# Performance work log

Measured on AMD Instinct MI355X. Metric: run time of the kernel, lower is better.

## Reference

```python
import jax, jax.numpy as jnp
import numpy as np

SCALE = 64 ** (-0.5)  # dim_head**-0.5; heads/dim_head otherwise unused in forward


def setup_inputs() -> dict:
    key = jax.random.key(0)
    ks = jax.random.split(key, 7)
    B, C, T = 8, 512, 4096
    s = C ** (-0.5)  # conv1d default init scale-ish
    x = jax.random.normal(ks[0], (B, C, T), dtype=jnp.float32)
    Wq = jax.random.normal(ks[1], (C, C), dtype=jnp.float32) * s
    bq = jax.random.normal(ks[2], (C,), dtype=jnp.float32) * s
    Wk = jax.random.normal(ks[3], (C, C), dtype=jnp.float32) * s
    bk = jax.random.normal(ks[4], (C,), dtype=jnp.float32) * s
    Wv = jax.random.normal(ks[5], (C, C), dtype=jnp.float32) * s
    bv = jax.random.normal(ks[6], (C,), dtype=jnp.float32) * s
    return {"x": x, "Wq": Wq, "bq": bq, "Wk": Wk, "bk": bk, "Wv": Wv, "bv": bv}


def reference(x, Wq, bq, Wk, bk, Wv, bv):
    # 1x1 Conv1d == per-timestep linear over channels: (o,c) x (b,c,t) -> (b,o,t)
    q = jnp.einsum('oc,bct->bot', Wq, x) + bq[None, :, None]
    k = jnp.einsum('oc,bct->bot', Wk, x) + bk[None, :, None]
    v = jnp.einsum('oc,bct->bot', Wv, x) + bv[None, :, None]
    # Channel-channel attention: dots (b, C, C); softmax over last (channel) axis
    dots = jnp.einsum('bct,bdt->bcd', q, k) * SCALE
    attn = jax.nn.softmax(dots, axis=-1)
    # (b,C,C) x (b,C,t) -> (b,C,t); dropout p=0 and to_out unused in original forward
    out = jnp.einsum('bcd,bdt->bct', attn, v)
    return out
```

## Files before the change

kernel.cpp:

```cpp
#include <hip/hip_runtime.h>

#define B_ 8
#define C_ 512
#define T_ 4096

typedef __attribute__((ext_vector_type(8))) __bf16 bf16x8;
typedef __attribute__((ext_vector_type(8))) _Float16 f16x8;
typedef __attribute__((ext_vector_type(8))) unsigned short u16x8;
typedef __attribute__((ext_vector_type(4))) float f32x4;

__device__ __forceinline__ unsigned short f2bf(float f) {
  unsigned int u = __float_as_uint(f);
  u += 0x7fffu + ((u >> 16) & 1u);
  return (unsigned short)(u >> 16);
}
__device__ __forceinline__ float bf2f(unsigned short h) {
  return __uint_as_float(((unsigned int)h) << 16);
}
__device__ __forceinline__ unsigned short f2h(float f) {
  return __builtin_bit_cast(unsigned short, (_Float16)f);
}

__device__ __forceinline__ void async16(unsigned short* ldsdst, const unsigned short* gsrc) {
  __builtin_amdgcn_global_load_lds(
      (__attribute__((address_space(1))) void*)(void*)const_cast<unsigned short*>(gsrc),
      (__attribute__((address_space(3))) void*)(void*)ldsdst,
      16, 0, 0);
}

template <bool F16>
__device__ __forceinline__ f32x4 mfma16(u16x8 a, u16x8 b, f32x4 c) {
  if constexpr (F16)
    return __builtin_amdgcn_mfma_f32_16x16x32_f16(
        __builtin_bit_cast(f16x8, a), __builtin_bit_cast(f16x8, b), c, 0, 0, 0);
  else
    return __builtin_amdgcn_mfma_f32_16x16x32_bf16(
        __builtin_bit_cast(bf16x8, a), __builtin_bit_cast(bf16x8, b), c, 0, 0, 0);
}

struct GemmP {
  const unsigned short* Ah; const unsigned short* Al; long sA; int lda;
  const unsigned short* Bh; const unsigned short* Bl; long sB; int ldb;
  float* Cf; unsigned short* Ch; unsigned short* Cl; long sC; int ldc;
  int kspan; int zparts;
  const float* rowv; const float* colv; const float* bq; const float* bk;
};

enum { EPI_F32 = 0, EPI_OUT = 1, EPI_DOTS = 2, EPI_SPLIT = 3, EPI_F16 = 4 };

template <int BM, int BN, int WM, int WN, bool SA, bool SB, int EPI, bool F16, bool TRI>
__global__ __launch_bounds__((BM / WM) * (BN / WN) * 64) void gemm_nt(GemmP g) {
  constexpr int KC = 64;
  constexpr int NWAVE = (BM / WM) * (BN / WN);
  constexpr int NT = NWAVE * 64;
  constexpr int ASZ = BM * KC, BSZ = BN * KC;
  constexpr int STAGE = (SA ? 2 : 1) * ASZ + (SB ? 2 : 1) * BSZ;
  constexpr int EPAD = BN + 4;
  constexpr int EPIB = 32 * EPAD * 4;
  constexpr int LDSB = (STAGE * 2 > EPIB) ? STAGE * 2 : EPIB;
  __shared__ alignas(16) char ldsraw[LDSB];
  unsigned short* lds = (unsigned short*)ldsraw;
  unsigned short* ldsAh = lds;
  unsigned short* ldsAl = lds + ASZ;
  unsigned short* ldsBh = lds + (SA ? 2 : 1) * ASZ;
  unsigned short* ldsBl = ldsBh + BSZ;

  const int tid = threadIdx.x;
  const int lane = tid & 63, wid = tid >> 6;
  constexpr int WNB = BN / WN;
  const int wm = wid / WNB, wn = wid % WNB;
  constexpr int MF = WM / 16, NF = WN / 16;

  int bm, bn;
  if constexpr (TRI) {
    const int t = blockIdx.x;
    const int tm = (t >= 6) ? 3 : (t >= 3) ? 2 : (t >= 1) ? 1 : 0;
    bm = tm; bn = t - (tm * (tm + 1)) / 2;
  } else {
    bm = blockIdx.x; bn = blockIdx.y;
  }
  const int z = blockIdx.z;
  const int b = z / g.zparts, kp = z - b * g.zparts;

  const unsigned short* Ah = g.Ah + (size_t)b * g.sA + (size_t)kp * g.kspan;
  const unsigned short* Al = SA ? (g.Al + (size_t)b * g.sA + (size_t)kp * g.kspan) : nullptr;
  const unsigned short* Bh = g.Bh + (size_t)b * g.sB + (size_t)kp * g.kspan;
  const unsigned short* Bl = SB ? (g.Bl + (size_t)b * g.sB + (size_t)kp * g.kspan) : nullptr;

  f32x4 acc[MF][NF] = {};

  const int kIters = g.kspan / KC;
  for (int kt = 0; kt < kIters; ++kt) {
    const int kb = kt * KC;
#pragma unroll
    for (int r = 0; r < ASZ / (8 * NT); ++r) {
      int idx = tid + r * NT;
      int row = idx >> 3, sl = idx & 7;
      int kc = (sl ^ (row & 7)) << 3;
      size_t goff = (size_t)(bm * BM + row) * g.lda + kb + kc;
      async16(&ldsAh[idx << 3], Ah + goff);
      if constexpr (SA) async16(&ldsAl[idx << 3], Al + goff);
    }
#pragma unroll
    for (int r = 0; r < BSZ / (8 * NT); ++r) {
      int idx = tid + r * NT;
      int row = idx >> 3, sl = idx & 7;
      int kc = (sl ^ (row & 7)) << 3;
      size_t goff = (size_t)(bn * BN + row) * g.ldb + kb + kc;
      async16(&ldsBh[idx << 3], Bh + goff);
      if constexpr (SB) async16(&ldsBl[idx << 3], Bl + goff);
    }
    __syncthreads();

    const int rsel = lane & 15, kq = lane >> 4;
#pragma unroll
    for (int ks = 0; ks < KC; ks += 32) {
      const int chunk = (ks >> 3) + kq;
      u16x8 afh[MF], afl[MF], bfh[NF], bfl[NF];
#pragma unroll
      for (int fm = 0; fm < MF; ++fm) {
        int row = wm * WM + fm * 16 + rsel;
        int ro = row * KC + ((chunk ^ (row & 7)) << 3);
        afh[fm] = *(const u16x8*)&ldsAh[ro];
        if constexpr (SA) afl[fm] = *(const u16x8*)&ldsAl[ro];
      }
#pragma unroll
      for (int fn = 0; fn < NF; ++fn) {
        int row = wn * WN + fn * 16 + rsel;
        int ro = row * KC + ((chunk ^ (row & 7)) << 3);
        bfh[fn] = *(const u16x8*)&ldsBh[ro];
        if constexpr (SB) bfl[fn] = *(const u16x8*)&ldsBl[ro];
      }
#pragma unroll
      for (int fm = 0; fm < MF; ++fm)
#pragma unroll
        for (int fn = 0; fn < NF; ++fn) {
          acc[fm][fn] = mfma16<F16>(afh[fm], bfh[fn], acc[fm][fn]);
          if constexpr (SB) acc[fm][fn] = mfma16<F16>(afh[fm], bfl[fn], acc[fm][fn]);
          if constexpr (SA) acc[fm][fn] = mfma16<F16>(afl[fm], bfh[fn], acc[fm][fn]);
        }
    }
    __syncthreads();
  }

  if constexpr (EPI == EPI_SPLIT || EPI == EPI_F16) {
#pragma unroll
    for (int fm = 0; fm < MF; ++fm)
#pragma unroll
      for (int fn = 0; fn < NF; ++fn)
#pragma unroll
        for (int r = 0; r < 4; ++r) {
          int i = bm * BM + wm * WM + fm * 16 + ((lane >> 4) << 2) + r;
          int j = bn * BN + wn * WN + fn * 16 + (lane & 15);
          float v = acc[fm][fn][r];
          size_t co = (size_t)z * g.sC + (size_t)i * g.ldc + j;
          if constexpr (EPI == EPI_SPLIT) {
            unsigned short h = f2bf(v);
            g.Ch[co] = h;
            g.Cl[co] = f2bf(v - bf2f(h));
          } else {
            g.Ch[co] = f2h(v);
          }
        }
  } else {
    float* eb = (float*)ldsraw;
#pragma unroll
    for (int ck = 0; ck < BM / 32; ++ck) {
      if (wm == (ck * 32) / WM) {
        const int fm0 = ((ck * 32) % WM) / 16;
#pragma unroll
        for (int fi = 0; fi < 2; ++fi) {
          int fm = fm0 + fi;
#pragma unroll
          for (int fn = 0; fn < NF; ++fn)
#pragma unroll
            for (int r = 0; r < 4; ++r) {
              int lrow = fi * 16 + ((lane >> 4) << 2) + r;
              int col = wn * WN + fn * 16 + (lane & 15);
              eb[lrow * EPAD + col] = acc[fm][fn][r];
            }
        }
      }
      __syncthreads();
#pragma unroll
      for (int it = 0; it < (32 * BN / 4) / NT; ++it) {
        int idx = it * NT + tid;
        int row = idx / (BN / 4), c4 = (idx % (BN / 4)) * 4;
        f32x4 v = *(f32x4*)&eb[row * EPAD + c4];
        int grow = bm * BM + ck * 32 + row;
        int j = bn * BN + c4;
        if constexpr (EPI == EPI_OUT) v = v + g.rowv[b * C_ + grow];
        if constexpr (EPI == EPI_DOTS) {
          f32x4 bkv = *(const f32x4*)&g.bk[j];
          f32x4 ksv = *(const f32x4*)&g.colv[b * C_ + j];
          float qsi = g.rowv[b * C_ + grow], bqi = g.bq[grow];
          v = 0.125f * (v + qsi * bkv + bqi * (ksv + 4096.f * bkv));
        }
        *(f32x4*)&g.Cf[(size_t)z * g.sC + (size_t)grow * g.ldc + j] = v;
      }
      __syncthreads();
    }
  }
}

#define NXB (64 * 8 * 8)
#define PAD 66
__global__ __launch_bounds__(256) void prep_fused(
    const float* __restrict__ x, const float* __restrict__ Wq,
    const float* __restrict__ Wk, const float* __restrict__ Wv,
    unsigned short* __restrict__ Xh, unsigned short* __restrict__ XhT,
    float* __restrict__ S, unsigned short* Wqh, unsigned short* Wql,
    unsigned short* Wkh, unsigned short* Wkl, unsigned short* WvT) {
  __shared__ unsigned short tile[64 * PAD];
  const int tid = threadIdx.x;
  if (blockIdx.x < NXB) {
    const int tl = blockIdx.x;
    const int t0 = (tl & 63) << 6, c0 = ((tl >> 6) & 7) << 6, b = tl >> 9;
    const float* xin = x + ((size_t)(b * C_ + c0)) * T_ + t0;
    unsigned short* xo = Xh + ((size_t)(b * C_ + c0)) * T_ + t0;
#pragma unroll
    for (int r = 0; r < 4; ++r) {
      int p = tid + r * 256;
      int row = p >> 4, c4 = (p & 15) << 2;
      float4 v = *(const float4*)&xin[(size_t)row * T_ + c4];
      unsigned short h0 = f2h(v.x), h1 = f2h(v.y), h2 = f2h(v.z), h3 = f2h(v.w);
      ushort4 hv; hv.x = h0; hv.y = h1; hv.z = h2; hv.w = h3;
      *(ushort4*)&xo[(size_t)row * T_ + c4] = hv;
      unsigned int lo = (unsigned int)h0 | ((unsigned int)h1 << 16);
      unsigned int hi = (unsigned int)h2 | ((unsigned int)h3 << 16);
      ((unsigned int*)&tile[row * PAD + c4])[0] = lo;
      ((unsigned int*)&tile[row * PAD + c4])[1] = hi;
      float s = v.x + v.y + v.z + v.w;
#pragma unroll
      for (int o = 1; o < 16; o <<= 1) s += __shfl_xor(s, o);
      if ((tid & 15) == 0) atomicAdd(&S[b * C_ + c0 + row], s);
    }
    __syncthreads();
#pragma unroll
    for (int r = 0; r < 2; ++r) {
      int idx = tid + r * 256;
      int trow = idx >> 3, cc = (idx & 7) << 3;
      unsigned short vals[8];
#pragma unroll
      for (int j = 0; j < 8; ++j) vals[j] = tile[(cc + j) * PAD + trow];
      *(uint4*)&XhT[((size_t)b * T_ + t0 + trow) * C_ + c0 + cc] = *(uint4*)vals;
    }
  } else {
    int i = (blockIdx.x - NXB) * 256 + tid;
    float q = Wq[i]; unsigned short qh = f2bf(q); Wqh[i] = qh; Wql[i] = f2bf(q - bf2f(qh));
    float k = Wk[i]; unsigned short kh = f2bf(k); Wkh[i] = kh; Wkl[i] = f2bf(k - bf2f(kh));
    float v = Wv[i]; int d = i >> 9, e = i & 511;
    WvT[(e << 9) + d] = f2h(v);
  }
}

__global__ __launch_bounds__(256) void combine_g(const float* __restrict__ gp,
                                                 unsigned short* __restrict__ gh,
                                                 unsigned short* __restrict__ gl) {
  __shared__ float tile[64 * 65];
  const int blk = blockIdx.x;
  const int b = blk >> 6, tr = (blk >> 3) & 7, tc = blk & 7;
  const bool mirror = (tr >> 1) < (tc >> 1);
  const int sr = mirror ? tc : tr, sc = mirror ? tr : tc;
  const float* src = gp + ((size_t)b << 21) + (size_t)(sr << 6) * 512 + (sc << 6);
  const int row = threadIdx.x >> 4, c4 = (threadIdx.x & 15) << 2;
  float vals[4][4];
#pragma unroll
  for (int rr = 0; rr < 4; ++rr) {
    const int r = row + rr * 16;
    f32x4 v = {};
#pragma unroll
    for (int p = 0; p < 8; ++p)
      v += *(const f32x4*)&src[((size_t)p << 18) + (size_t)r * 512 + c4];
    if (mirror) {
#pragma unroll
      for (int k = 0; k < 4; ++k) tile[r * 65 + c4 + k] = v[k];
    } else {
#pragma unroll
      for (int k = 0; k < 4; ++k) vals[rr][k] = v[k];
    }
  }
  if (mirror) {
    __syncthreads();
#pragma unroll
    for (int rr = 0; rr < 4; ++rr) {
      const int r = row + rr * 16;
#pragma unroll
      for (int k = 0; k < 4; ++k) vals[rr][k] = tile[(c4 + k) * 65 + r];
    }
  }
  unsigned short* ghp = gh + ((size_t)b << 18) + (size_t)(tr << 6) * 512 + (tc << 6);
  unsigned short* glp = gl + ((size_t)b << 18) + (size_t)(tr << 6) * 512 + (tc << 6);
#pragma unroll
  for (int rr = 0; rr < 4; ++rr) {
    const int r = row + rr * 16;
    ushort4 h, l;
    h.x = f2bf(vals[rr][0]); l.x = f2bf(vals[rr][0] - bf2f(h.x));
    h.y = f2bf(vals[rr][1]); l.y = f2bf(vals[rr][1] - bf2f(h.y));
    h.z = f2bf(vals[rr][2]); l.z = f2bf(vals[rr][2] - bf2f(h.z));
    h.w = f2bf(vals[rr][3]); l.w = f2bf(vals[rr][3] - bf2f(h.w));
    *(ushort4*)&ghp[(size_t)r * 512 + c4] = h;
    *(ushort4*)&glp[(size_t)r * 512 + c4] = l;
  }
}

__global__ __launch_bounds__(256) void qs_ks(const float* __restrict__ Wq, const float* __restrict__ Wk,
                                             const float* __restrict__ s, float* __restrict__ qs,
                                             float* __restrict__ ks) {
  int lane = threadIdx.x & 63, wid = threadIdx.x >> 6;
  int gi = blockIdx.x * 4 + wid;
  int b = gi >> 9, i = gi & 511;
  const float* sv = s + (b << 9);
  const float* wqr = Wq + (size_t)i * C_;
  const float* wkr = Wk + (size_t)i * C_;
  float aq = 0.f, ak = 0.f;
#pragma unroll
  for (int c = lane; c < C_; c += 64) {
    float sc = sv[c];
    aq += wqr[c] * sc;
    ak += wkr[c] * sc;
  }
#pragma unroll
  for (int o = 32; o > 0; o >>= 1) { aq += __shfl_down(aq, o); ak += __shfl_down(ak, o); }
  if (lane == 0) { qs[gi] = aq; ks[gi] = ak; }
}

__global__ __launch_bounds__(256) void softmax_rows(const float* __restrict__ logits,
                                                    const float* __restrict__ bv,
                                                    unsigned short* __restrict__ attn,
                                                    float* __restrict__ ab) {
  const int row = blockIdx.x;
  const int tid = threadIdx.x, lane = tid & 63, wid = tid >> 6;
  const float* L = logits + (size_t)row * C_;
  float v0 = L[tid], v1 = L[tid + 256];
  __shared__ float red[4];
  float m = fmaxf(v0, v1);
#pragma unroll
  for (int o = 32; o > 0; o >>= 1) m = fmaxf(m, __shfl_down(m, o));
  if (lane == 0) red[wid] = m;
  __syncthreads();
  m = fmaxf(fmaxf(red[0], red[1]), fmaxf(red[2], red[3]));
  __syncthreads();
  float e0 = __expf(v0 - m), e1 = __expf(v1 - m);
  float sum = e0 + e1;
#pragma unroll
  for (int o = 32; o > 0; o >>= 1) sum += __shfl_down(sum, o);
  if (lane == 0) red[wid] = sum;
  __syncthreads();
  sum = red[0] + red[1] + red[2] + red[3];
  float inv = 1.f / sum;
  float a0 = e0 * inv, a1 = e1 * inv;
  unsigned short* ar = attn + (size_t)row * C_;
  ar[tid] = f2h(a0);
  ar[tid + 256] = f2h(a1);
  float abv = a0 * bv[tid] + a1 * bv[tid + 256];
  __syncthreads();
#pragma unroll
  for (int o = 32; o > 0; o >>= 1) abv += __shfl_down(abv, o);
  if (lane == 0) red[wid] = abv;
  __syncthreads();
  if (tid == 0) ab[row] = red[0] + red[1] + red[2] + red[3];
}

extern "C" void kernel_launch(void* const* d_in, const int* in_sizes, int n_in,
                              void* d_out, int out_size, void* d_ws, size_t ws_size,
                              hipStream_t stream) {
  const float* x  = (const float*)d_in[0];
  const float* Wq = (const float*)d_in[1];
  const float* bq = (const float*)d_in[2];
  const float* Wk = (const float*)d_in[3];
  const float* bk = (const float*)d_in[4];
  const float* Wv = (const float*)d_in[5];
  const float* bv = (const float*)d_in[6];
  float* out = (float*)d_out;

  char* ws = (char*)d_ws;
  size_t off = 0;
  auto alloc = [&](size_t bytes) {
    char* p = ws + off;
    off += (bytes + 255) & ~(size_t)255;
    return p;
  };
  const size_t XSZ = (size_t)B_ * C_ * T_;
  const size_t GSZ = (size_t)B_ * C_ * C_;

  unsigned short* Xh  = (unsigned short*)alloc(XSZ * 2);
  unsigned short* XhT = (unsigned short*)alloc(XSZ * 2);
  float* Gpart = (float*)alloc((size_t)8 * GSZ * 4);
  unsigned short* Gh = (unsigned short*)alloc(GSZ * 2);
  unsigned short* Gl = (unsigned short*)alloc(GSZ * 2);
  unsigned short* Ph = (unsigned short*)alloc(GSZ * 2);
  unsigned short* Pl = (unsigned short*)alloc(GSZ * 2);
  float* Logits = (float*)alloc(GSZ * 4);
  unsigned short* Attn = (unsigned short*)alloc(GSZ * 2);
  unsigned short* Mh = (unsigned short*)alloc(GSZ * 2);
  unsigned short* Wqh = (unsigned short*)alloc((size_t)C_ * C_ * 2);
  unsigned short* Wql = (unsigned short*)alloc((size_t)C_ * C_ * 2);
  unsigned short* Wkh = (unsigned short*)alloc((size_t)C_ * C_ * 2);
  unsigned short* Wkl = (unsigned short*)alloc((size_t)C_ * C_ * 2);
  unsigned short* WvT = (unsigned short*)alloc((size_t)C_ * C_ * 2);
  float* S  = (float*)alloc((size_t)B_ * C_ * 4);
  float* Qs = (float*)alloc((size_t)B_ * C_ * 4);
  float* Ks = (float*)alloc((size_t)B_ * C_ * 4);
  float* Ab = (float*)alloc((size_t)B_ * C_ * 4);

  hipMemsetAsync(S, 0, (size_t)B_ * C_ * 4, stream);
  prep_fused<<<NXB + C_ * C_ / 256, 256, 0, stream>>>(x, Wq, Wk, Wv, Xh, XhT, S,
                                                      Wqh, Wql, Wkh, Wkl, WvT);
  qs_ks<<<B_ * C_ / 4, 256, 0, stream>>>(Wq, Wk, S, Qs, Ks);

  {
    GemmP p = {};
    p.Ah = Xh; p.sA = (long)C_ * T_; p.lda = T_;
    p.Bh = Xh; p.sB = (long)C_ * T_; p.ldb = T_;
    p.Cf = Gpart; p.sC = (long)C_ * C_; p.ldc = C_;
    p.kspan = T_ / 8; p.zparts = 8;
    gemm_nt<128, 128, 32, 64, false, false, EPI_F32, true, true>
        <<<dim3(10, 1, 64), 512, 0, stream>>>(p);
  }
  combine_g<<<B_ * 64, 256, 0, stream>>>(Gpart, Gh, Gl);

  {
    GemmP p = {};
    p.Ah = Wqh; p.Al = Wql; p.sA = 0; p.lda = C_;
    p.Bh = Gh; p.Bl = Gl; p.sB = (long)C_ * C_; p.ldb = C_;
    p.Ch = Ph; p.Cl = Pl; p.sC = (long)C_ * C_; p.ldc = C_;
    p.kspan = C_; p.zparts = 1;
    gemm_nt<64, 64, 32, 32, true, true, EPI_SPLIT, false, false>
        <<<dim3(8, 8, 8), 256, 0, stream>>>(p);
  }
  {
    GemmP p = {};
    p.Ah = Ph; p.Al = Pl; p.sA = (long)C_ * C_; p.lda = C_;
    p.Bh = Wkh; p.Bl = Wkl; p.sB = 0; p.ldb = C_;
    p.Cf = Logits; p.sC = (long)C_ * C_; p.ldc = C_;
    p.kspan = C_; p.zparts = 1;
    p.rowv = Qs; p.colv = Ks; p.bq = bq; p.bk = bk;
    gemm_nt<64, 64, 32, 32, true, true, EPI_DOTS, false, false>
        <<<dim3(8, 8, 8), 256, 0, stream>>>(p);
  }
  softmax_rows<<<B_ * C_, 256, 0, stream>>>(Logits, bv, Attn, Ab);
  {
    GemmP p = {};
    p.Ah = Attn; p.sA = (long)C_ * C_; p.lda = C_;
    p.Bh = WvT; p.sB = 0; p.ldb = C_;
    p.Ch = Mh; p.sC = (long)C_ * C_; p.ldc = C_;
    p.kspan = C_; p.zparts = 1;
    gemm_nt<64, 64, 32, 32, false, false, EPI_F16, true, false>
        <<<dim3(8, 8, 8), 256, 0, stream>>>(p);
  }
  {
    GemmP p = {};
    p.Ah = Mh; p.sA = (long)C_ * C_; p.lda = C_;
    p.Bh = XhT; p.sB = (long)C_ * T_; p.ldb = C_;
    p.Cf = out; p.sC = (long)C_ * T_; p.ldc = T_;
    p.kspan = C_; p.zparts = 1;
    p.rowv = Ab;
    gemm_nt<128, 128, 64, 64, false, false, EPI_OUT, true, false>
        <<<dim3(C_ / 128, T_ / 128, B_), 256, 0, stream>>>(p);
  }
  (void)in_sizes; (void)n_in; (void)out_size; (void)ws_size;
}
```

Baseline: 255.1 us.

## Swizzle block indices across XCDs and enlarge output GEMM tile

Replaces the 3D grids of the Gram GEMM and the output GEMM with flat 1D grids, decoding the block index so the low 3 bits pick the batch or column group. The intent is that blocks landing on the same XCD under round-robin dispatch share operand data, improving per-XCD L2 reuse. combine_g gets the same batch-in-low-bits remapping. The output GEMM also moves from 128x128 tiles with 256 threads to 128x256 tiles with 512 threads, which raises per-block LDS use and may lower occupancy.

```diff
diff --git a/kernel.cpp b/kernel.cpp
--- a/kernel.cpp
+++ b/kernel.cpp
@@ -48,7 +48,7 @@
 
 enum { EPI_F32 = 0, EPI_OUT = 1, EPI_DOTS = 2, EPI_SPLIT = 3, EPI_F16 = 4 };
 
-template <int BM, int BN, int WM, int WN, bool SA, bool SB, int EPI, bool F16, bool TRI>
+template <int BM, int BN, int WM, int WN, bool SA, bool SB, int EPI, bool F16, int SWZ>
 __global__ __launch_bounds__((BM / WM) * (BN / WN) * 64) void gemm_nt(GemmP g) {
   constexpr int KC = 64;
   constexpr int NWAVE = (BM / WM) * (BN / WN);
@@ -71,15 +71,24 @@
   const int wm = wid / WNB, wn = wid % WNB;
   constexpr int MF = WM / 16, NF = WN / 16;
 
-  int bm, bn;
-  if constexpr (TRI) {
-    const int t = blockIdx.x;
-    const int tm = (t >= 6) ? 3 : (t >= 3) ? 2 : (t >= 1) ? 1 : 0;
-    bm = tm; bn = t - (tm * (tm + 1)) / 2;
+  int bm, bn, z;
+  if constexpr (SWZ == 1) {
+    const int blk = blockIdx.x;
+    const int r = blk & 7, q = blk >> 3;
+    const int tri = q % 10, zq = q / 10;
+    const int tm = (tri >= 6) ? 3 : (tri >= 3) ? 2 : (tri >= 1) ? 1 : 0;
+    bm = tm; bn = tri - (tm * (tm + 1)) / 2;
+    z = zq * 8 + r;
+  } else if constexpr (SWZ == 2) {
+    const int blk = blockIdx.x;
+    const int r = blk & 7, q = blk >> 3;
+    bm = q & 3;
+    const int w = q >> 2;
+    bn = ((w & 1) << 3) + r;
+    z = w >> 1;
   } else {
-    bm = blockIdx.x; bn = blockIdx.y;
-  }
-  const int z = blockIdx.z;
+    bm = blockIdx.x; bn = blockIdx.y; z = blockIdx.z;
+  }
   const int b = z / g.zparts, kp = z - b * g.zparts;
 
   const unsigned short* Ah = g.Ah + (size_t)b * g.sA + (size_t)kp * g.kspan;
@@ -259,7 +268,8 @@
                                                  unsigned short* __restrict__ gl) {
   __shared__ float tile[64 * 65];
   const int blk = blockIdx.x;
-  const int b = blk >> 6, tr = (blk >> 3) & 7, tc = blk & 7;
+  const int b = blk & 7, q = blk >> 3;
+  const int tr = q >> 3, tc = q & 7;
   const bool mirror = (tr >> 1) < (tc >> 1);
   const int sr = mirror ? tc : tr, sc = mirror ? tr : tc;
   const float* src = gp + ((size_t)b << 21) + (size_t)(sr << 6) * 512 + (sc << 6);
@@ -415,8 +425,8 @@
     p.Bh = Xh; p.sB = (long)C_ * T_; p.ldb = T_;
     p.Cf = Gpart; p.sC = (long)C_ * C_; p.ldc = C_;
     p.kspan = T_ / 8; p.zparts = 8;
-    gemm_nt<128, 128, 32, 64, false, false, EPI_F32, true, true>
-        <<<dim3(10, 1, 64), 512, 0, stream>>>(p);
+    gemm_nt<128, 128, 32, 64, false, false, EPI_F32, true, 1>
+        <<<640, 512, 0, stream>>>(p);
   }
   combine_g<<<B_ * 64, 256, 0, stream>>>(Gpart, Gh, Gl);
 
@@ -426,7 +436,7 @@
     p.Bh = Gh; p.Bl = Gl; p.sB = (long)C_ * C_; p.ldb = C_;
     p.Ch = Ph; p.Cl = Pl; p.sC = (long)C_ * C_; p.ldc = C_;
     p.kspan = C_; p.zparts = 1;
-    gemm_nt<64, 64, 32, 32, true, true, EPI_SPLIT, false, false>
+    gemm_nt<64, 64, 32, 32, true, true, EPI_SPLIT, false, 0>
         <<<dim3(8, 8, 8), 256, 0, stream>>>(p);
   }
   {
@@ -436,7 +446,7 @@
     p.Cf = Logits; p.sC = (long)C_ * C_; p.ldc = C_;
     p.kspan = C_; p.zparts = 1;
     p.rowv = Qs; p.colv = Ks; p.bq = bq; p.bk = bk;
-    gemm_nt<64, 64, 32, 32, true, true, EPI_DOTS, false, false>
+    gemm_nt<64, 64, 32, 32, true, true, EPI_DOTS, false, 0>
         <<<dim3(8, 8, 8), 256, 0, stream>>>(p);
   }
   softmax_rows<<<B_ * C_, 256, 0, stream>>>(Logits, bv, Attn, Ab);
@@ -446,7 +456,7 @@
     p.Bh = WvT; p.sB = 0; p.ldb = C_;
     p.Ch = Mh; p.sC = (long)C_ * C_; p.ldc = C_;
     p.kspan = C_; p.zparts = 1;
-    gemm_nt<64, 64, 32, 32, false, false, EPI_F16, true, false>
+    gemm_nt<64, 64, 32, 32, false, false, EPI_F16, true, 0>
         <<<dim3(8, 8, 8), 256, 0, stream>>>(p);
   }
   {
@@ -456,8 +466,8 @@
     p.Cf = out; p.sC = (long)C_ * T_; p.ldc = T_;
     p.kspan = C_; p.zparts = 1;
     p.rowv = Ab;
-    gemm_nt<128, 128, 64, 64, false, false, EPI_OUT, true, false>
-        <<<dim3(C_ / 128, T_ / 128, B_), 256, 0, stream>>>(p);
+    gemm_nt<128, 256, 64, 64, false, false, EPI_OUT, true, 2>
+        <<<512, 512, 0, stream>>>(p);
   }
   (void)in_sizes; (void)n_in; (void)out_size; (void)ws_size;
 }
```

New measurement: 234.0 us. 1.09x faster.
